# Optimization experiments

Measured on AMD Instinct MI355X. Metric: run time of the kernel, lower is better.

Reference implementation:

```python
import jax, jax.numpy as jnp
import numpy as np

TEMPERATURE = 0.1
NUM_CLASSES = 21
L2_EPS = 1e-12   # torch F.normalize eps
NEG = -1e9       # masking value for invalid (absent-class) logit slots


def setup_inputs() -> dict:
    key = jax.random.key(0)
    k1, k2 = jax.random.split(key)
    features = jax.random.normal(k1, (16, 512, 64, 64), dtype=jnp.float32)
    labels = jax.random.randint(k2, (16, 513, 513), 0, NUM_CLASSES, dtype=jnp.int32)
    return {"features": features, "labels": labels}


def reference(features, labels):
    B, D, H, W = features.shape
    C = NUM_CLASSES
    # torch: F.interpolate(labels.float()[:,None], (H,W), mode='bilinear').squeeze(1).long()
    lab = jax.image.resize(labels.astype(jnp.float32)[:, None], (B, 1, H, W),
                           method="bilinear", antialias=False)
    lab = lab[:, 0].astype(jnp.int32)                     # [B,H,W]

    # per-image, per-class masked feature pooling (segment reduce)
    masks = (lab[:, None, :, :] == jnp.arange(C)[None, :, None, None]).astype(features.dtype)  # [B,C,H,W]
    sums = jnp.einsum('bdhw,bchw->bcd', features, masks)  # [B,C,D]
    norms = jnp.linalg.norm(sums, axis=-1, keepdims=True)
    protos = sums / jnp.maximum(norms, L2_EPS)            # normalized prototypes [B,C,D]
    pres = masks.sum((2, 3)) > 0                          # [B,C] class present in image

    # all pairwise prototype dots: S[c,e,i,j] = <proto[i,c], proto[j,e]> / T
    S = jnp.einsum('icd,jed->ceij', protos, protos) / TEMPERATURE  # [C,C,B,B]
    presT = pres.T                                        # [C,B]
    valid = presT[:, None, :, None] & presT[None, :, None, :]       # [C,C,B,B]
    masked = jnp.where(valid, S, NEG)

    idx = jnp.arange(C)
    diag = masked[idx, idx]                               # [C,B,B] positive block S[c,c]
    dvalid = valid[idx, idx]                              # [C,B,B]

    # logits for class c = concat(p_block, all n_blocks) -> diag block appears twice
    lse_diag = jax.nn.logsumexp(diag, axis=(1, 2))        # [C]
    lse_all = jax.nn.logsumexp(masked, axis=(1, 2, 3))    # [C]
    lse = jnp.logaddexp(lse_diag, lse_all)                # [C]

    cnt = dvalid.sum((1, 2))
    pos_mean = jnp.where(dvalid, diag, 0.0).sum((1, 2)) / jnp.maximum(cnt, 1)

    cls_present = pres.any(0)                             # [C]
    loss = jnp.sum(jnp.where(cls_present, lse - pos_mean, 0.0))
    return loss
```

## Files before the change

kernel.cpp:

```cpp
#include <hip/hip_runtime.h>
#include <cstdint>
#include <cstddef>

#define NUM_C 21
#define NROW 336
#define N2   (NROW * NROW)

__global__ __launch_bounds__(256) void k1_resize_hist(const int* __restrict__ labels,
                                                      uint8_t* __restrict__ lab,
                                                      int* __restrict__ countsPart,
                                                      float* __restrict__ out) {
    int b = blockIdx.x >> 4, strip = blockIdx.x & 15;
    if (blockIdx.x == 0 && threadIdx.x == 0) out[0] = 0.0f;
    __shared__ int hist[NUM_C];
    if (threadIdx.x < NUM_C) hist[threadIdx.x] = 0;
    __syncthreads();

    int p = strip * 256 + threadIdx.x;
    int y = p >> 6, x = p & 63;
    const int* L = labels + (size_t)b * 263169;
    float sy = (y + 0.5f) * 8.015625f - 0.5f;
    float sx = (x + 0.5f) * 8.015625f - 0.5f;
    int y0 = (int)sy; float fy = sy - (float)y0;
    int x0 = (int)sx; float fx = sx - (float)x0;
    const int* r0 = L + y0 * 513 + x0;
    float L00 = (float)r0[0],   L01 = (float)r0[1];
    float L10 = (float)r0[513], L11 = (float)r0[514];
    float v0 = (1.0f - fx) * L00 + fx * L01;
    float v1 = (1.0f - fx) * L10 + fx * L11;
    float val = (1.0f - fy) * v0 + fy * v1;
    int c = (int)val;
    lab[b * 4096 + p] = (uint8_t)c;
    atomicAdd(&hist[c], 1);
    __syncthreads();
    if (threadIdx.x < NUM_C) countsPart[blockIdx.x * NUM_C + threadIdx.x] = hist[threadIdx.x];
}

__global__ __launch_bounds__(256) void k2_sums(const float* __restrict__ feat,
                                               const uint8_t* __restrict__ lab,
                                               float* __restrict__ sums) {
    int b  = blockIdx.x >> 7;
    int dg = blockIdx.x & 127;
    int t = threadIdx.x;
    int wv = t >> 6, lane = t & 63;
    __shared__ uint32_t lab4[1024];
    __shared__ float accum[4][NUM_C * 64];

    const uint32_t* labSrc = (const uint32_t*)(lab + b * 4096);
#pragma unroll
    for (int q = 0; q < 4; ++q) lab4[t + 256 * q] = labSrc[t + 256 * q];
    float* accFlat = &accum[0][0];
#pragma unroll
    for (int q = 0; q < NUM_C; ++q) accFlat[t + 256 * q] = 0.0f;
    __syncthreads();

    int d = dg * 4 + wv;
    const float4* f4 = (const float4*)(feat + ((size_t)(b * 512 + d)) * 4096);
    float* acc = accum[wv];
#pragma unroll 4
    for (int it = 0; it < 16; ++it) {
        int p4 = it * 64 + lane;
        float4 v = f4[p4];
        uint32_t l4 = lab4[p4];
        acc[(l4 & 255u) * 64 + lane]         += v.x;
        acc[((l4 >> 8) & 255u) * 64 + lane]  += v.y;
        acc[((l4 >> 16) & 255u) * 64 + lane] += v.z;
        acc[(l4 >> 24) * 64 + lane]          += v.w;
    }
    for (int c = 0; c < NUM_C; ++c) {
        float v = acc[c * 64 + lane];
#pragma unroll
        for (int off = 32; off >= 1; off >>= 1) v += __shfl_xor(v, off, 64);
        if (lane == 0) sums[(size_t)(c * 16 + b) * 512 + d] = v;
    }
}

__global__ __launch_bounds__(64) void k4_gram(const float* __restrict__ sums,
                                              float* __restrict__ gpart) {
    int row0 = blockIdx.x * 32, col0 = blockIdx.y * 32, k0 = blockIdx.z * 64;
    __shared__ float A[32 * 66], Bt[32 * 66];
    int t = threadIdx.x;
    int row = t >> 1, kk0 = (t & 1) * 32;
#pragma unroll
    for (int q = 0; q < 8; ++q) {
        int kk = kk0 + q * 4;
        int ra = row0 + row, rb = col0 + row;
        float4 va = (ra < NROW) ? *(const float4*)&sums[(size_t)ra * 512 + k0 + kk]
                                : make_float4(0.f, 0.f, 0.f, 0.f);
        float4 vb = (rb < NROW) ? *(const float4*)&sums[(size_t)rb * 512 + k0 + kk]
                                : make_float4(0.f, 0.f, 0.f, 0.f);
        *(float2*)&A[row * 66 + kk]      = make_float2(va.x, va.y);
        *(float2*)&A[row * 66 + kk + 2]  = make_float2(va.z, va.w);
        *(float2*)&Bt[row * 66 + kk]     = make_float2(vb.x, vb.y);
        *(float2*)&Bt[row * 66 + kk + 2] = make_float2(vb.z, vb.w);
    }
    __syncthreads();
    int ty = t >> 3, tx = t & 7;
    float acc[4][4] = {};
    for (int kk = 0; kk < 64; kk += 2) {
        float2 a[4], bb[4];
#pragma unroll
        for (int u = 0; u < 4; ++u) {
            a[u]  = *(const float2*)&A[(ty * 4 + u) * 66 + kk];
            bb[u] = *(const float2*)&Bt[(tx * 4 + u) * 66 + kk];
        }
#pragma unroll
        for (int u = 0; u < 4; ++u)
#pragma unroll
            for (int v = 0; v < 4; ++v)
                acc[u][v] += a[u].x * bb[v].x + a[u].y * bb[v].y;
    }
    float* gp = gpart + (size_t)blockIdx.z * N2;
#pragma unroll
    for (int u = 0; u < 4; ++u) {
        int r1 = row0 + ty * 4 + u;
        if (r1 >= NROW) continue;
#pragma unroll
        for (int v = 0; v < 4; ++v) {
            int r2 = col0 + tx * 4 + v;
            if (r2 < NROW) gp[(size_t)r1 * NROW + r2] = acc[u][v];
        }
    }
}

__global__ __launch_bounds__(512) void k5_loss(const float* __restrict__ gpart,
                                               const int* __restrict__ countsPart,
                                               float* __restrict__ out) {
    int c = blockIdx.x, t = threadIdx.x;
    int wv = t >> 6, lane = t & 63;
    __shared__ float invnL[NROW];
    __shared__ uint8_t presL[NROW];
    __shared__ float redE[8], redD[8], redL[8];

    for (int r = t; r < NROW; r += 512) {
        float ss = 0.0f;
#pragma unroll
        for (int s = 0; s < 8; ++s) ss += gpart[(size_t)s * N2 + (size_t)r * 337];
        invnL[r] = 1.0f / fmaxf(sqrtf(ss), 1e-12f);
        int img = r & 15, cls = r >> 4;
        int cnt = 0;
#pragma unroll
        for (int s = 0; s < 16; ++s) cnt += countsPart[(img * 16 + s) * NUM_C + cls];
        presL[r] = cnt > 0 ? 1 : 0;
    }
    __syncthreads();

    int nc = 0;
#pragma unroll
    for (int j = 0; j < 16; ++j) nc += presL[c * 16 + j];
    if (nc == 0) return;

    float eS = 0.0f, dE = 0.0f, dL = 0.0f;
    for (int idx = t; idx < 16 * NROW; idx += 512) {
        int i = idx / NROW, r2 = idx - i * NROW;
        int r1 = c * 16 + i;
        float g = 0.0f;
#pragma unroll
        for (int s = 0; s < 8; ++s) g += gpart[(size_t)s * N2 + (size_t)r1 * NROW + r2];
        if (presL[r1] && presL[r2]) {
            float sv = g * invnL[r1] * invnL[r2] * 10.0f;
            float e = expf(sv - 10.0f);
            eS += e;
            if ((r2 >> 4) == c) { dE += e; dL += sv; }
        }
    }
#pragma unroll
    for (int off = 32; off >= 1; off >>= 1) {
        eS += __shfl_xor(eS, off, 64);
        dE += __shfl_xor(dE, off, 64);
        dL += __shfl_xor(dL, off, 64);
    }
    if (lane == 0) { redE[wv] = eS; redD[wv] = dE; redL[wv] = dL; }
    __syncthreads();
    if (t == 0) {
        float E = 0, D = 0, Ln = 0;
#pragma unroll
        for (int w = 0; w < 8; ++w) { E += redE[w]; D += redD[w]; Ln += redL[w]; }
        float lse = 10.0f + logf(E + D);
        float posMean = Ln / (float)(nc * nc);
        atomicAdd(out, lse - posMean);
    }
}

extern "C" void kernel_launch(void* const* d_in, const int* in_sizes, int n_in,
                              void* d_out, int out_size, void* d_ws, size_t ws_size,
                              hipStream_t stream) {
    const float* features = (const float*)d_in[0];
    const int* labels = (const int*)d_in[1];
    char* ws = (char*)d_ws;

    uint8_t* lab    = (uint8_t*)ws;
    int* countsPart = (int*)(ws + 65536);
    float* sums     = (float*)(ws + 65536 + 21504);
    float* gpart    = (float*)(ws + 65536 + 21504 + 688128);
    float* out      = (float*)d_out;

    k1_resize_hist<<<256, 256, 0, stream>>>(labels, lab, countsPart, out);
    k2_sums<<<2048, 256, 0, stream>>>(features, lab, sums);
    k4_gram<<<dim3(11, 11, 8), 64, 0, stream>>>(sums, gpart);
    k5_loss<<<21, 512, 0, stream>>>(gpart, countsPart, out);
}
```

Baseline: 231.1 us.

## Vectorize LDS init/stores, use LDS atomics in sums, widen loss block

```diff
diff --git a/kernel.cpp b/kernel.cpp
--- a/kernel.cpp
+++ b/kernel.cpp
@@ -46,12 +46,13 @@
     __shared__ uint32_t lab4[1024];
     __shared__ float accum[4][NUM_C * 64];
 
-    const uint32_t* labSrc = (const uint32_t*)(lab + b * 4096);
-#pragma unroll
-    for (int q = 0; q < 4; ++q) lab4[t + 256 * q] = labSrc[t + 256 * q];
-    float* accFlat = &accum[0][0];
-#pragma unroll
-    for (int q = 0; q < NUM_C; ++q) accFlat[t + 256 * q] = 0.0f;
+    ((uint4*)lab4)[t] = ((const uint4*)(lab + b * 4096))[t];
+
+    float4* accF4 = (float4*)&accum[0][0];
+    float4 z4 = make_float4(0.f, 0.f, 0.f, 0.f);
+#pragma unroll
+    for (int q = 0; q < 5; ++q) accF4[t + 256 * q] = z4;
+    if (t < 64) accF4[t + 1280] = z4;
     __syncthreads();
 
     int d = dg * 4 + wv;
@@ -62,16 +63,24 @@
         int p4 = it * 64 + lane;
         float4 v = f4[p4];
         uint32_t l4 = lab4[p4];
-        acc[(l4 & 255u) * 64 + lane]         += v.x;
-        acc[((l4 >> 8) & 255u) * 64 + lane]  += v.y;
-        acc[((l4 >> 16) & 255u) * 64 + lane] += v.z;
-        acc[(l4 >> 24) * 64 + lane]          += v.w;
-    }
-    for (int c = 0; c < NUM_C; ++c) {
-        float v = acc[c * 64 + lane];
-#pragma unroll
-        for (int off = 32; off >= 1; off >>= 1) v += __shfl_xor(v, off, 64);
-        if (lane == 0) sums[(size_t)(c * 16 + b) * 512 + d] = v;
+        atomicAdd(&acc[(l4 & 255u) * 64 + lane],         v.x);
+        atomicAdd(&acc[((l4 >> 8) & 255u) * 64 + lane],  v.y);
+        atomicAdd(&acc[((l4 >> 16) & 255u) * 64 + lane], v.z);
+        atomicAdd(&acc[(l4 >> 24) * 64 + lane],          v.w);
+    }
+    __syncthreads();
+
+    if (t < 84) {
+        int c = t >> 2, dwv = t & 3;
+        int l = t & 63;
+        const float4* a4 = (const float4*)(accum[dwv] + c * 64);
+        float s = 0.f;
+#pragma unroll
+        for (int k = 0; k < 16; ++k) {
+            float4 vv = a4[(l + k) & 15];
+            s += (vv.x + vv.y) + (vv.z + vv.w);
+        }
+        sums[(size_t)(c * 16 + b) * 512 + dg * 4 + dwv] = s;
     }
 }
 
@@ -115,24 +124,28 @@
     for (int u = 0; u < 4; ++u) {
         int r1 = row0 + ty * 4 + u;
         if (r1 >= NROW) continue;
-#pragma unroll
-        for (int v = 0; v < 4; ++v) {
-            int r2 = col0 + tx * 4 + v;
-            if (r2 < NROW) gp[(size_t)r1 * NROW + r2] = acc[u][v];
-        }
-    }
-}
-
-__global__ __launch_bounds__(512) void k5_loss(const float* __restrict__ gpart,
-                                               const int* __restrict__ countsPart,
-                                               float* __restrict__ out) {
+        int r2 = col0 + tx * 4;
+        if (r2 + 3 < NROW) {
+            *(float4*)&gp[(size_t)r1 * NROW + r2] =
+                make_float4(acc[u][0], acc[u][1], acc[u][2], acc[u][3]);
+        } else {
+#pragma unroll
+            for (int v = 0; v < 4; ++v)
+                if (r2 + v < NROW) gp[(size_t)r1 * NROW + r2 + v] = acc[u][v];
+        }
+    }
+}
+
+__global__ __launch_bounds__(1024) void k5_loss(const float* __restrict__ gpart,
+                                                const int* __restrict__ countsPart,
+                                                float* __restrict__ out) {
     int c = blockIdx.x, t = threadIdx.x;
     int wv = t >> 6, lane = t & 63;
     __shared__ float invnL[NROW];
     __shared__ uint8_t presL[NROW];
-    __shared__ float redE[8], redD[8], redL[8];
-
-    for (int r = t; r < NROW; r += 512) {
+    __shared__ float redE[16], redD[16], redL[16];
+
+    for (int r = t; r < NROW; r += 1024) {
         float ss = 0.0f;
 #pragma unroll
         for (int s = 0; s < 8; ++s) ss += gpart[(size_t)s * N2 + (size_t)r * 337];
@@ -151,7 +164,7 @@
     if (nc == 0) return;
 
     float eS = 0.0f, dE = 0.0f, dL = 0.0f;
-    for (int idx = t; idx < 16 * NROW; idx += 512) {
+    for (int idx = t; idx < 16 * NROW; idx += 1024) {
         int i = idx / NROW, r2 = idx - i * NROW;
         int r1 = c * 16 + i;
         float g = 0.0f;
@@ -175,7 +188,7 @@
     if (t == 0) {
         float E = 0, D = 0, Ln = 0;
 #pragma unroll
-        for (int w = 0; w < 8; ++w) { E += redE[w]; D += redD[w]; Ln += redL[w]; }
+        for (int w = 0; w < 16; ++w) { E += redE[w]; D += redD[w]; Ln += redL[w]; }
         float lse = 10.0f + logf(E + D);
         float posMean = Ln / (float)(nc * nc);
         atomicAdd(out, lse - posMean);
@@ -198,5 +211,5 @@
     k1_resize_hist<<<256, 256, 0, stream>>>(labels, lab, countsPart, out);
     k2_sums<<<2048, 256, 0, stream>>>(features, lab, sums);
     k4_gram<<<dim3(11, 11, 8), 64, 0, stream>>>(sums, gpart);
-    k5_loss<<<21, 512, 0, stream>>>(gpart, countsPart, out);
-}
+    k5_loss<<<21, 1024, 0, stream>>>(gpart, countsPart, out);
+}
```

New measurement: 343.8 us. 48.8% more time.
